# Kernel tuning notes

Measured on AMD Instinct MI355X. Metric: run time of the kernel, lower is better.

## Reference

```python
import math
import jax, jax.numpy as jnp
import numpy as np

TOP_K = 2
N_EXP = 8
EVAL_CAPACITY_FACTOR = 2.0  # eval mode (module not training)
MIN_CAPACITY = 4


def _capacity(num_tokens):
    cap = math.floor(TOP_K * EVAL_CAPACITY_FACTOR * num_tokens / N_EXP)
    cap += cap % 2
    return max(cap, MIN_CAPACITY)


def setup_inputs() -> dict:
    key = jax.random.key(0)
    k1, k2 = jax.random.split(key)
    x = jax.random.normal(k1, (2, 2048, 1024), dtype=jnp.float32)
    w_g = jax.random.normal(k2, (8, 1024), dtype=jnp.float32) * 0.02
    return {"x": x, "w_g": w_g}


def reference(x, w_g):
    B, T, C = x.shape
    num_tokens = B * T
    cap = _capacity(num_tokens)  # static, derived from shapes

    # gating logits [B,T,E]
    logits = jnp.einsum('btc,ec->bte', x, w_g)

    # top-k + masked softmax (non-top-k logits -> -inf)
    top_logits, top_idx = jax.lax.top_k(logits, TOP_K)  # [B,T,K]
    masked = jnp.full_like(logits, -jnp.inf)
    masked = jnp.put_along_axis(masked, top_idx, top_logits, axis=-1, inplace=False)
    router_probs = jax.nn.softmax(masked, axis=-1)  # [B,T,E]

    # one-hot expert mask, ordered (k-major then token) for capacity ranking
    exp_mask = jax.nn.one_hot(top_idx, N_EXP, dtype=jnp.int32)       # [B,T,K,E]
    exp_mask = exp_mask.reshape(num_tokens, TOP_K, N_EXP)
    exp_mask = jnp.transpose(exp_mask, (1, 0, 2))                     # [K,tokens,E]

    # position of each assignment within its expert's queue
    exp_rank = jnp.cumsum(exp_mask.reshape(TOP_K * num_tokens, N_EXP), axis=0) - 1
    exp_rank = exp_rank.reshape(TOP_K, num_tokens, N_EXP)

    # drop assignments beyond capacity
    exp_mask = exp_mask * (exp_rank < cap).astype(jnp.int32)
    used_capacity = jnp.sum(exp_mask, axis=(0, 1))                    # [E]

    # per-assignment slot index [K,tokens]
    exp_rank = jnp.sum(exp_mask * exp_rank, axis=-1)

    rp = router_probs.reshape(num_tokens, N_EXP)[None, :, :]          # [1,tokens,E]
    exp_weights = exp_mask.astype(rp.dtype) * rp                      # [K,tokens,E]

    # one-hot over capacity slots -> combine weights [tokens,E,cap]
    exp_rank_sc = jax.nn.one_hot(exp_rank, cap, dtype=rp.dtype)       # [K,tokens,cap]
    cb_weight = jnp.sum(exp_weights[:, :, :, None] * exp_rank_sc[:, :, None, :], axis=0)
    sec_mask = cb_weight.astype(bool)
    return (used_capacity, cb_weight, sec_mask)
```

## Files before the change

kernel.cpp:

```cpp
#include <hip/hip_runtime.h>
#include <math.h>

#define TOKENS   4096
#define CDIM     1024
#define NEXP     8
#define CAP      2048
#define OUT_OFS  8
#define PER_OUT  (TOKENS * NEXP * CAP)

__global__ __launch_bounds__(256) void gating_kernel(const float* __restrict__ x,
                                                     const float* __restrict__ wg,
                                                     int*   __restrict__ top1,
                                                     int*   __restrict__ top2,
                                                     float* __restrict__ p1,
                                                     float* __restrict__ p2) {
    __shared__ float swg[NEXP * CDIM];
    for (int i = threadIdx.x; i < NEXP * CDIM / 4; i += 256)
        ((float4*)swg)[i] = ((const float4*)wg)[i];
    __syncthreads();

    const int wave = threadIdx.x >> 6;
    const int lane = threadIdx.x & 63;
    const int tok  = blockIdx.x * 4 + wave;
    const float* xr = x + (size_t)tok * CDIM;

    float acc[NEXP];
#pragma unroll
    for (int e = 0; e < NEXP; ++e) acc[e] = 0.f;

#pragma unroll
    for (int i = 0; i < CDIM / 64; ++i) {
        const float xv = xr[lane + 64 * i];
#pragma unroll
        for (int e = 0; e < NEXP; ++e)
            acc[e] = fmaf(xv, swg[e * CDIM + lane + 64 * i], acc[e]);
    }
#pragma unroll
    for (int e = 0; e < NEXP; ++e) {
        float v = acc[e];
#pragma unroll
        for (int s = 32; s >= 1; s >>= 1) v += __shfl_xor(v, s, 64);
        acc[e] = v;
    }

    if (lane == 0) {
        int e1 = 0; float l1 = acc[0];
#pragma unroll
        for (int e = 1; e < NEXP; ++e)
            if (acc[e] > l1) { l1 = acc[e]; e1 = e; }
        int e2 = -1; float l2 = -INFINITY;
#pragma unroll
        for (int e = 0; e < NEXP; ++e)
            if (e != e1 && acc[e] > l2) { l2 = acc[e]; e2 = e; }
        const float ex = expf(l2 - l1);
        const float denom = 1.f + ex;
        top1[tok] = e1;
        top2[tok] = e2;
        p1[tok] = 1.f / denom;
        p2[tok] = ex / denom;
    }
}

__global__ __launch_bounds__(64) void scan_kernel(const int* __restrict__ top1,
                                                  const int* __restrict__ top2,
                                                  int* __restrict__ r1,
                                                  int* __restrict__ r2,
                                                  float* __restrict__ out) {
    const int lane = threadIdx.x;
    const int* __restrict__ src = (lane < 32) ? (top1 + lane * 128)
                                              : (top2 + (lane - 32) * 128);
    int4 a[32];
#pragma unroll
    for (int i = 0; i < 32; ++i) a[i] = ((const int4*)src)[i];

    unsigned long long cnt = 0ull;
#pragma unroll
    for (int i = 0; i < 32; ++i) {
        cnt += 1ull << (a[i].x << 3);
        cnt += 1ull << (a[i].y << 3);
        cnt += 1ull << (a[i].z << 3);
        cnt += 1ull << (a[i].w << 3);
    }
    int c[NEXP];
#pragma unroll
    for (int e = 0; e < NEXP; ++e) c[e] = (int)((cnt >> (e * 8)) & 0xff);

    int off[NEXP], tot[NEXP];
#pragma unroll
    for (int e = 0; e < NEXP; ++e) {
        int v = c[e];
#pragma unroll
        for (int s = 1; s <= 32; s <<= 1) {
            const int u = __shfl_up(v, s, 64);
            if (lane >= s) v += u;
        }
        off[e] = v - c[e];
        tot[e] = __shfl(v, 63, 64);
    }

    int* __restrict__ dst = (lane < 32) ? (r1 + lane * 128)
                                        : (r2 + (lane - 32) * 128);
#pragma unroll
    for (int i = 0; i < 32; ++i) {
        int4 r;
        int e, rr;
        e = a[i].x; rr = 0;
#pragma unroll
        for (int ee = 0; ee < NEXP; ++ee) if (e == ee) { rr = off[ee]; off[ee] = rr + 1; }
        r.x = rr;
        e = a[i].y; rr = 0;
#pragma unroll
        for (int ee = 0; ee < NEXP; ++ee) if (e == ee) { rr = off[ee]; off[ee] = rr + 1; }
        r.y = rr;
        e = a[i].z; rr = 0;
#pragma unroll
        for (int ee = 0; ee < NEXP; ++ee) if (e == ee) { rr = off[ee]; off[ee] = rr + 1; }
        r.z = rr;
        e = a[i].w; rr = 0;
#pragma unroll
        for (int ee = 0; ee < NEXP; ++ee) if (e == ee) { rr = off[ee]; off[ee] = rr + 1; }
        r.w = rr;
        ((int4*)dst)[i] = r;
    }

    if (lane < NEXP)
        out[lane] = (float)(tot[lane] < CAP ? tot[lane] : CAP);
}

__global__ __launch_bounds__(256) void scatter_kernel(const int* __restrict__ top1,
                                                      const int* __restrict__ top2,
                                                      const float* __restrict__ p1,
                                                      const float* __restrict__ p2,
                                                      const int* __restrict__ r1,
                                                      const int* __restrict__ r2,
                                                      float* __restrict__ out) {
    const int a = blockIdx.x * 256 + threadIdx.x;
    const int k = (a >= TOKENS);
    const int t = a & (TOKENS - 1);
    const int e = k ? top2[t] : top1[t];
    const int r = k ? r2[t] : r1[t];
    const float p = k ? p2[t] : p1[t];
    if (r < CAP) {
        const size_t idx = ((size_t)t * NEXP + e) * CAP + r;
        out[OUT_OFS + idx] = p;
        out[OUT_OFS + (size_t)PER_OUT + idx] = (p != 0.f) ? 1.f : 0.f;
    }
}

extern "C" void kernel_launch(void* const* d_in, const int* in_sizes, int n_in,
                              void* d_out, int out_size, void* d_ws, size_t ws_size,
                              hipStream_t stream) {
    const float* x  = (const float*)d_in[0];
    const float* wg = (const float*)d_in[1];
    float* out = (float*)d_out;

    int*   top1 = (int*)d_ws;
    int*   top2 = top1 + TOKENS;
    int*   r1   = top2 + TOKENS;
    int*   r2   = r1 + TOKENS;
    float* p1   = (float*)(r2 + TOKENS);
    float* p2   = p1 + TOKENS;

    hipMemsetAsync(out, 0, (size_t)(2 * PER_OUT + OUT_OFS) * sizeof(float), stream);

    gating_kernel<<<TOKENS / 4, 256, 0, stream>>>(x, wg, top1, top2, p1, p2);

    scan_kernel<<<1, 64, 0, stream>>>(top1, top2, r1, r2, out);

    scatter_kernel<<<2 * TOKENS / 256, 256, 0, stream>>>(top1, top2, p1, p2, r1, r2, out);
}
```

Before: 114.4 us.

## Fuse output zeroing with gating and merge scan with scatter into one block

Replaces the memset with a custom zero-fill that runs in extra blocks of the gating kernel, so the large fill and the gating GEMV share one launch. Gating now handles four tokens per wave and reads the gate weights straight from global memory instead of staging them in LDS. The scan and scatter kernels are merged into one single-block kernel that keeps ranks in shared memory, removing a launch and a global round trip. The risk is that the scatter of 8192 assignments now runs on a single block, and the zero-fill's bandwidth depends on a hand-written kernel instead of the runtime memset.

```diff
diff --git a/kernel.cpp b/kernel.cpp
--- a/kernel.cpp
+++ b/kernel.cpp
@@ -7,143 +7,154 @@
 #define CAP      2048
 #define OUT_OFS  8
 #define PER_OUT  (TOKENS * NEXP * CAP)
+#define N4TOTAL  ((2 * PER_OUT + OUT_OFS) / 4)
 
-__global__ __launch_bounds__(256) void gating_kernel(const float* __restrict__ x,
-                                                     const float* __restrict__ wg,
-                                                     int*   __restrict__ top1,
-                                                     int*   __restrict__ top2,
-                                                     float* __restrict__ p1,
-                                                     float* __restrict__ p2) {
-    __shared__ float swg[NEXP * CDIM];
-    for (int i = threadIdx.x; i < NEXP * CDIM / 4; i += 256)
-        ((float4*)swg)[i] = ((const float4*)wg)[i];
-    __syncthreads();
+#define GATE_BLOCKS   256
+#define TOK_PER_WAVE  4
+#define FILL_BLOCKS   ((N4TOTAL + 511) / 512)
+
+__global__ __launch_bounds__(256) void fill_gate_kernel(const float* __restrict__ x,
+                                                        const float* __restrict__ wg,
+                                                        int*   __restrict__ top1,
+                                                        int*   __restrict__ top2,
+                                                        float* __restrict__ p1,
+                                                        float* __restrict__ p2,
+                                                        float4* __restrict__ out4) {
+    if (blockIdx.x >= GATE_BLOCKS) {
+        const int i = (blockIdx.x - GATE_BLOCKS) * 512 + threadIdx.x;
+        const float4 z = make_float4(0.f, 0.f, 0.f, 0.f);
+        if (i < N4TOTAL) out4[i] = z;
+        const int i2 = i + 256;
+        if (i2 < N4TOTAL) out4[i2] = z;
+        return;
+    }
 
     const int wave = threadIdx.x >> 6;
     const int lane = threadIdx.x & 63;
-    const int tok  = blockIdx.x * 4 + wave;
-    const float* xr = x + (size_t)tok * CDIM;
 
-    float acc[NEXP];
+    for (int tt = 0; tt < TOK_PER_WAVE; ++tt) {
+        const int tok = (blockIdx.x * 4 + wave) * TOK_PER_WAVE + tt;
+        const float* xr = x + (size_t)tok * CDIM;
+
+        float acc[NEXP];
 #pragma unroll
-    for (int e = 0; e < NEXP; ++e) acc[e] = 0.f;
+        for (int e = 0; e < NEXP; ++e) acc[e] = 0.f;
 
 #pragma unroll
-    for (int i = 0; i < CDIM / 64; ++i) {
-        const float xv = xr[lane + 64 * i];
+        for (int i = 0; i < CDIM / 64; ++i) {
+            const float xv = xr[lane + 64 * i];
 #pragma unroll
-        for (int e = 0; e < NEXP; ++e)
-            acc[e] = fmaf(xv, swg[e * CDIM + lane + 64 * i], acc[e]);
-    }
+            for (int e = 0; e < NEXP; ++e)
+                acc[e] = fmaf(xv, wg[e * CDIM + lane + 64 * i], acc[e]);
+        }
 #pragma unroll
-    for (int e = 0; e < NEXP; ++e) {
-        float v = acc[e];
+        for (int e = 0; e < NEXP; ++e) {
+            float v = acc[e];
 #pragma unroll
-        for (int s = 32; s >= 1; s >>= 1) v += __shfl_xor(v, s, 64);
-        acc[e] = v;
-    }
+            for (int s = 32; s >= 1; s >>= 1) v += __shfl_xor(v, s, 64);
+            acc[e] = v;
+        }
 
-    if (lane == 0) {
-        int e1 = 0; float l1 = acc[0];
+        if (lane == 0) {
+            int e1 = 0; float l1 = acc[0];
 #pragma unroll
-        for (int e = 1; e < NEXP; ++e)
-            if (acc[e] > l1) { l1 = acc[e]; e1 = e; }
-        int e2 = -1; float l2 = -INFINITY;
+            for (int e = 1; e < NEXP; ++e)
+                if (acc[e] > l1) { l1 = acc[e]; e1 = e; }
+            int e2 = -1; float l2 = -INFINITY;
 #pragma unroll
-        for (int e = 0; e < NEXP; ++e)
-            if (e != e1 && acc[e] > l2) { l2 = acc[e]; e2 = e; }
-        const float ex = expf(l2 - l1);
-        const float denom = 1.f + ex;
-        top1[tok] = e1;
-        top2[tok] = e2;
-        p1[tok] = 1.f / denom;
-        p2[tok] = ex / denom;
+            for (int e = 0; e < NEXP; ++e)
+                if (e != e1 && acc[e] > l2) { l2 = acc[e]; e2 = e; }
+            const float ex = expf(l2 - l1);
+            const float denom = 1.f + ex;
+            top1[tok] = e1;
+            top2[tok] = e2;
+            p1[tok] = 1.f / denom;
+            p2[tok] = ex / denom;
+        }
     }
 }
 
-__global__ __launch_bounds__(64) void scan_kernel(const int* __restrict__ top1,
-                                                  const int* __restrict__ top2,
-                                                  int* __restrict__ r1,
-                                                  int* __restrict__ r2,
-                                                  float* __restrict__ out) {
-    const int lane = threadIdx.x;
-    const int* __restrict__ src = (lane < 32) ? (top1 + lane * 128)
-                                              : (top2 + (lane - 32) * 128);
-    int4 a[32];
+__global__ __launch_bounds__(256) void scan_scatter_kernel(const int* __restrict__ top1,
+                                                           const int* __restrict__ top2,
+                                                           const float* __restrict__ p1,
+                                                           const float* __restrict__ p2,
+                                                           float* __restrict__ out) {
+    __shared__ int sr[2 * TOKENS];
+    const int tid = threadIdx.x;
+
+    if (tid < 64) {
+        const int lane = tid;
+        const int* __restrict__ src = (lane < 32) ? (top1 + lane * 128)
+                                                  : (top2 + (lane - 32) * 128);
+        int4 a[32];
 #pragma unroll
-    for (int i = 0; i < 32; ++i) a[i] = ((const int4*)src)[i];
+        for (int i = 0; i < 32; ++i) a[i] = ((const int4*)src)[i];
 
-    unsigned long long cnt = 0ull;
+        unsigned long long cnt = 0ull;
 #pragma unroll
-    for (int i = 0; i < 32; ++i) {
-        cnt += 1ull << (a[i].x << 3);
-        cnt += 1ull << (a[i].y << 3);
-        cnt += 1ull << (a[i].z << 3);
-        cnt += 1ull << (a[i].w << 3);
+        for (int i = 0; i < 32; ++i) {
+            cnt += 1ull << (a[i].x << 3);
+            cnt += 1ull << (a[i].y << 3);
+            cnt += 1ull << (a[i].z << 3);
+            cnt += 1ull << (a[i].w << 3);
+        }
+        int c[NEXP];
+#pragma unroll
+        for (int e = 0; e < NEXP; ++e) c[e] = (int)((cnt >> (e * 8)) & 0xff);
+
+        int off[NEXP], tot[NEXP];
+#pragma unroll
+        for (int e = 0; e < NEXP; ++e) {
+            int v = c[e];
+#pragma unroll
+            for (int s = 1; s <= 32; s <<= 1) {
+                const int u = __shfl_up(v, s, 64);
+                if (lane >= s) v += u;
+            }
+            off[e] = v - c[e];
+            tot[e] = __shfl(v, 63, 64);
+        }
+
+        int4* __restrict__ dst = (int4*)sr + lane * 32;
+#pragma unroll
+        for (int i = 0; i < 32; ++i) {
+            int4 r;
+            int e, rr;
+            e = a[i].x; rr = 0;
+#pragma unroll
+            for (int ee = 0; ee < NEXP; ++ee) if (e == ee) { rr = off[ee]; off[ee] = rr + 1; }
+            r.x = rr;
+            e = a[i].y; rr = 0;
+#pragma unroll
+            for (int ee = 0; ee < NEXP; ++ee) if (e == ee) { rr = off[ee]; off[ee] = rr + 1; }
+            r.y = rr;
+            e = a[i].z; rr = 0;
+#pragma unroll
+            for (int ee = 0; ee < NEXP; ++ee) if (e == ee) { rr = off[ee]; off[ee] = rr + 1; }
+            r.z = rr;
+            e = a[i].w; rr = 0;
+#pragma unroll
+            for (int ee = 0; ee < NEXP; ++ee) if (e == ee) { rr = off[ee]; off[ee] = rr + 1; }
+            r.w = rr;
+            dst[i] = r;
+        }
+
+        if (lane < NEXP)
+            out[lane] = (float)(tot[lane] < CAP ? tot[lane] : CAP);
     }
-    int c[NEXP];
-#pragma unroll
-    for (int e = 0; e < NEXP; ++e) c[e] = (int)((cnt >> (e * 8)) & 0xff);
+    __syncthreads();
 
-    int off[NEXP], tot[NEXP];
-#pragma unroll
-    for (int e = 0; e < NEXP; ++e) {
-        int v = c[e];
-#pragma unroll
-        for (int s = 1; s <= 32; s <<= 1) {
-            const int u = __shfl_up(v, s, 64);
-            if (lane >= s) v += u;
+    for (int a = tid; a < 2 * TOKENS; a += 256) {
+        const int k = (a >= TOKENS);
+        const int t = a & (TOKENS - 1);
+        const int e = k ? top2[t] : top1[t];
+        const int r = sr[a];
+        const float p = k ? p2[t] : p1[t];
+        if (r < CAP) {
+            const size_t idx = ((size_t)t * NEXP + e) * CAP + r;
+            out[OUT_OFS + idx] = p;
+            out[OUT_OFS + (size_t)PER_OUT + idx] = (p != 0.f) ? 1.f : 0.f;
         }
-        off[e] = v - c[e];
-        tot[e] = __shfl(v, 63, 64);
-    }
-
-    int* __restrict__ dst = (lane < 32) ? (r1 + lane * 128)
-                                        : (r2 + (lane - 32) * 128);
-#pragma unroll
-    for (int i = 0; i < 32; ++i) {
-        int4 r;
-        int e, rr;
-        e = a[i].x; rr = 0;
-#pragma unroll
-        for (int ee = 0; ee < NEXP; ++ee) if (e == ee) { rr = off[ee]; off[ee] = rr + 1; }
-        r.x = rr;
-        e = a[i].y; rr = 0;
-#pragma unroll
-        for (int ee = 0; ee < NEXP; ++ee) if (e == ee) { rr = off[ee]; off[ee] = rr + 1; }
-        r.y = rr;
-        e = a[i].z; rr = 0;
-#pragma unroll
-        for (int ee = 0; ee < NEXP; ++ee) if (e == ee) { rr = off[ee]; off[ee] = rr + 1; }
-        r.z = rr;
-        e = a[i].w; rr = 0;
-#pragma unroll
-        for (int ee = 0; ee < NEXP; ++ee) if (e == ee) { rr = off[ee]; off[ee] = rr + 1; }
-        r.w = rr;
-        ((int4*)dst)[i] = r;
-    }
-
-    if (lane < NEXP)
-        out[lane] = (float)(tot[lane] < CAP ? tot[lane] : CAP);
-}
-
-__global__ __launch_bounds__(256) void scatter_kernel(const int* __restrict__ top1,
-                                                      const int* __restrict__ top2,
-                                                      const float* __restrict__ p1,
-                                                      const float* __restrict__ p2,
-                                                      const int* __restrict__ r1,
-                                                      const int* __restrict__ r2,
-                                                      float* __restrict__ out) {
-    const int a = blockIdx.x * 256 + threadIdx.x;
-    const int k = (a >= TOKENS);
-    const int t = a & (TOKENS - 1);
-    const int e = k ? top2[t] : top1[t];
-    const int r = k ? r2[t] : r1[t];
-    const float p = k ? p2[t] : p1[t];
-    if (r < CAP) {
-        const size_t idx = ((size_t)t * NEXP + e) * CAP + r;
-        out[OUT_OFS + idx] = p;
-        out[OUT_OFS + (size_t)PER_OUT + idx] = (p != 0.f) ? 1.f : 0.f;
     }
 }
 
@@ -156,16 +167,11 @@
 
     int*   top1 = (int*)d_ws;
     int*   top2 = top1 + TOKENS;
-    int*   r1   = top2 + TOKENS;
-    int*   r2   = r1 + TOKENS;
-    float* p1   = (float*)(r2 + TOKENS);
+    float* p1   = (float*)(top2 + TOKENS);
     float* p2   = p1 + TOKENS;
 
-    hipMemsetAsync(out, 0, (size_t)(2 * PER_OUT + OUT_OFS) * sizeof(float), stream);
+    fill_gate_kernel<<<GATE_BLOCKS + FILL_BLOCKS, 256, 0, stream>>>(
+        x, wg, top1, top2, p1, p2, (float4*)out);
 
-    gating_kernel<<<TOKENS / 4, 256, 0, stream>>>(x, wg, top1, top2, p1, p2);
-
-    scan_kernel<<<1, 64, 0, stream>>>(top1, top2, r1, r2, out);
-
-    scatter_kernel<<<2 * TOKENS / 256, 256, 0, stream>>>(top1, top2, p1, p2, r1, r2, out);
+    scan_scatter_kernel<<<1, 256, 0, stream>>>(top1, top2, p1, p2, out);
 }
```

Result: slower. 132.2 us (+15.6%).
